# Performance work log

Hardware: AMD Instinct MI355X
Metric: run time of the kernel (lower is better)

## Reference

```python
import jax, jax.numpy as jnp
import numpy as np

DIM = 1024
NUM_ATT = 8
NUM_HEADS = 16
HEAD_DIM = DIM // NUM_HEADS
ROPE_BASE = 10000.0
NEG_INF = -1e9


def _rope(x):
    # x: [B, H, L, hd]; torchtune-style interleaved RoPE applied along the sequence axis.
    B, H, L, hd = x.shape
    pos = jnp.arange(L, dtype=jnp.float32)
    inv_freq = 1.0 / (ROPE_BASE ** (jnp.arange(0, hd, 2, dtype=jnp.float32) / hd))
    ang = pos[:, None] * inv_freq[None, :]          # [L, hd/2]
    cos = jnp.cos(ang)[None, None]                  # [1,1,L,hd/2]
    sin = jnp.sin(ang)[None, None]
    xr = x.reshape(B, H, L, hd // 2, 2)
    x0, x1 = xr[..., 0], xr[..., 1]
    out = jnp.stack([x0 * cos - x1 * sin, x1 * cos + x0 * sin], axis=-1)
    return out.reshape(B, H, L, hd).astype(x.dtype)


def setup_inputs() -> dict:
    key = jax.random.key(0)
    ks = jax.random.split(key, 7)
    B, L = 32, 512
    x = jax.random.normal(ks[0], (B, L, DIM), dtype=jnp.float32)
    s = 0.02  # init scale for numerical sanity (init choice, not math)
    query_projs = jax.random.normal(ks[1], (NUM_ATT, DIM, DIM), dtype=jnp.float32) * s
    key_projs = jax.random.normal(ks[2], (NUM_ATT, DIM, DIM), dtype=jnp.float32) * s
    value_projs = jax.random.normal(ks[3], (NUM_ATT, DIM, DIM), dtype=jnp.float32) * s
    out_projs = jax.random.normal(ks[4], (NUM_ATT, DIM, DIM), dtype=jnp.float32) * s
    router_w = jax.random.normal(ks[5], (DIM, NUM_ATT), dtype=jnp.float32) * s
    router_b = jnp.zeros((NUM_ATT,), dtype=jnp.float32)
    return {"x": x, "query_projs": query_projs, "key_projs": key_projs,
            "value_projs": value_projs, "out_projs": out_projs,
            "router_w": router_w, "router_b": router_b}


def reference(x, query_projs, key_projs, value_projs, out_projs, router_w, router_b):
    B, L, D = x.shape
    H, hd = NUM_HEADS, HEAD_DIM
    scale = hd ** -0.5

    # top-1 routing on mean-pooled tokens
    logits = x.mean(axis=1) @ router_w + router_b       # [B, E]
    attn_probs = jax.nn.softmax(logits, axis=-1)
    routes = jnp.argmax(attn_probs, axis=-1)            # [B] int

    # per-batch weight gather (the memory-bound irregular access) + bmm
    qw = query_projs[routes]                             # [B, D, D]
    kw = key_projs[routes]
    vw = value_projs[routes]
    q = jnp.einsum('bld,bde->ble', x, qw)
    k = jnp.einsum('bld,bde->ble', x, kw)
    v = jnp.einsum('bld,bde->ble', x, vw)

    q = q.reshape(B, L, H, hd).transpose(0, 2, 1, 3)     # [B,H,L,hd]
    k = k.reshape(B, L, H, hd).transpose(0, 2, 1, 3)
    v = v.reshape(B, L, H, hd).transpose(0, 2, 1, 3)

    q = _rope(q)
    k = _rope(k)

    scores = jnp.einsum('bhld,bhmd->bhlm', q, k) * scale  # [B,H,L,L]
    causal = jnp.triu(jnp.ones((L, L), dtype=bool), k=1)  # True above diag = masked
    scores = jnp.where(causal[None, None], NEG_INF, scores)
    attn = jax.nn.softmax(scores, axis=-1)
    out = jnp.einsum('bhlm,bhmd->bhld', attn, v)          # [B,H,L,hd]
    out = out.transpose(0, 2, 1, 3).reshape(B, L, D)

    ow = out_projs[routes]                                # [B, D, D]
    out = jnp.einsum('bld,bde->ble', out, ow)
    return out, attn_probs
```

## Files before the change

### kernel.cpp

```cpp
#include <hip/hip_runtime.h>


typedef __attribute__((ext_vector_type(8))) short bf16x8;
typedef __attribute__((ext_vector_type(4))) float f32x4;

typedef const __attribute__((address_space(1))) unsigned short* gas_t;
typedef __attribute__((address_space(3))) unsigned short* las_t;

#define OFF_PART   (0ull)
#define OFF_ROUTES (2ull << 20)
#define OFF_XB     (3ull << 20)
#define OFF_WT     (40ull << 20)
#define OFF_QKV    (112ull << 20)

__device__ __forceinline__ unsigned short f2bf(float f){
  unsigned int u = __float_as_uint(f);
  u += 0x7fffu + ((u >> 16) & 1u);
  return (unsigned short)(u >> 16);
}


__global__ void meanpool_kernel(const float* __restrict__ x, float* __restrict__ part,
                                unsigned short* __restrict__ xb){
  const int b = blockIdx.x, lc = blockIdx.y, t = threadIdx.x;
  const size_t base = ((size_t)b*512 + lc*32)*1024;
  const float* xs = x + base;
  unsigned short* xo = xb + base;
  float4 a = {0.f, 0.f, 0.f, 0.f};
  for (int l = 0; l < 32; ++l){
    const float4 v = *(const float4*)(xs + l*1024 + t*4);
    a.x += v.x; a.y += v.y; a.z += v.z; a.w += v.w;
    ushort4 pk;
    pk.x = f2bf(v.x); pk.y = f2bf(v.y); pk.z = f2bf(v.z); pk.w = f2bf(v.w);
    *(ushort4*)(xo + l*1024 + t*4) = pk;
  }
  *(float4*)(part + ((size_t)b*16 + lc)*1024 + t*4) = a;
}


__global__ void router_kernel(const float* __restrict__ part,
                              const float* __restrict__ rw,
                              const float* __restrict__ rbias,
                              float* __restrict__ probs,
                              int* __restrict__ routes){
  const int b = blockIdx.x, t = threadIdx.x;
  const int lane = t & 63, wave = t >> 6;
  __shared__ float wred[4][8];
  float p[8] = {0.f,0.f,0.f,0.f,0.f,0.f,0.f,0.f};
  #pragma unroll
  for (int k = 0; k < 4; ++k){
    const int d = t + k*256;
    float s = 0.f;
    #pragma unroll
    for (int lc = 0; lc < 16; ++lc)
      s += part[((size_t)b*16 + lc)*1024 + d];
    s *= (1.0f/512.0f);
    const float4 w0 = *(const float4*)(rw + d*8);
    const float4 w1 = *(const float4*)(rw + d*8 + 4);
    p[0] = fmaf(s, w0.x, p[0]); p[1] = fmaf(s, w0.y, p[1]);
    p[2] = fmaf(s, w0.z, p[2]); p[3] = fmaf(s, w0.w, p[3]);
    p[4] = fmaf(s, w1.x, p[4]); p[5] = fmaf(s, w1.y, p[5]);
    p[6] = fmaf(s, w1.z, p[6]); p[7] = fmaf(s, w1.w, p[7]);
  }
  #pragma unroll
  for (int off = 1; off < 64; off <<= 1)
    #pragma unroll
    for (int e = 0; e < 8; ++e)
      p[e] += __shfl_xor(p[e], off, 64);
  if (lane == 0){
    #pragma unroll
    for (int e = 0; e < 8; ++e) wred[wave][e] = p[e];
  }
  __syncthreads();
  if (t == 0){
    float lg[8], mx = -3e38f; int am = 0;
    #pragma unroll
    for (int e = 0; e < 8; ++e){
      lg[e] = wred[0][e] + wred[1][e] + wred[2][e] + wred[3][e] + rbias[e];
      if (lg[e] > mx){ mx = lg[e]; am = e; }
    }
    float sum = 0.f, ex[8];
    #pragma unroll
    for (int e = 0; e < 8; ++e){ ex[e] = __expf(lg[e] - mx); sum += ex[e]; }
    const float inv = 1.0f / sum;
    #pragma unroll
    for (int e = 0; e < 8; ++e) probs[b*8 + e] = ex[e] * inv;
    routes[b] = am;
  }
}


__global__ void wcast_kernel(const float* __restrict__ qw, const float* __restrict__ kw,
                             const float* __restrict__ vw, const float* __restrict__ ow,
                             unsigned short* __restrict__ Wt){
  __shared__ float tile[64][65];
  const int z = blockIdx.z;
  const float* Wm = (z < 8 ? qw : z < 16 ? kw : z < 24 ? vw : ow) + (size_t)(z & 7)*1024*1024;
  unsigned short* Wo = Wt + (size_t)z*1024*1024;
  const int t = threadIdx.x;
  const int r = t >> 4;
  const int c4 = t & 15;
  const int gx = blockIdx.x*64, gy = blockIdx.y*64;
  #pragma unroll
  for (int k = 0; k < 4; ++k){
    const int rr = r + 16*k;
    const float4 v = *(const float4*)(Wm + (size_t)(gy + rr)*1024 + gx + c4*4);
    tile[rr][c4*4+0] = v.x; tile[rr][c4*4+1] = v.y;
    tile[rr][c4*4+2] = v.z; tile[rr][c4*4+3] = v.w;
  }
  __syncthreads();
  #pragma unroll
  for (int k = 0; k < 4; ++k){
    const int rr = r + 16*k;
    ushort4 pk;
    pk.x = f2bf(tile[c4*4+0][rr]); pk.y = f2bf(tile[c4*4+1][rr]);
    pk.z = f2bf(tile[c4*4+2][rr]); pk.w = f2bf(tile[c4*4+3][rr]);
    *(ushort4*)(Wo + (size_t)(gx + rr)*1024 + gy + c4*4) = pk;
  }
}


template<int MODE>
__global__ __launch_bounds__(512, 2) void gemm_kernel(
    const unsigned short* __restrict__ A,
    const unsigned short* __restrict__ Wt,
    const int* __restrict__ routes,
    unsigned short* __restrict__ qkvout,
    float* __restrict__ outf,
    int pp)
{
  __shared__ __align__(16) unsigned short As[2][256*64];
  __shared__ __align__(16) unsigned short Bs[2][256*64];

  const int f = blockIdx.x + blockIdx.y*8;
  const int wg = (f & 7)*32 + (f >> 3);
  const int b    = wg >> 3;
  const int tile = wg & 7;
  const int m0 = (tile >> 2)*256;
  const int n0 = (tile & 3)*256;

  const int route = routes[b];
  const unsigned short* Ab = A + (size_t)b*512*1024;
  const unsigned short* Wb = Wt + (size_t)((MODE == 0) ? (pp*8 + route) : route)*1024*1024;

  const int t = threadIdx.x;
  const int lane = t & 63;
  const int wave = t >> 6;
  const int wm = (wave >> 2)*128;
  const int wn = (wave & 3)*64;
  const int quad = lane >> 4;
  const int ln = lane & 15;

  const int srow = t >> 3;
  const int schA = (t & 7) ^ (srow & 7);
  const int schB = (t & 7) ^ ((t >> 5) & 7);
  const unsigned short* gA0 = Ab + (size_t)(m0 + srow)*1024 + schA*8;
  const unsigned short* gB0 = Wb + (size_t)(n0 + srow)*1024 + schB*8;

  const int w8 = ln & 7;
  const int aO0 = (wm + ln)*64 + ((quad    ) ^ w8)*8;
  const int aO1 = (wm + ln)*64 + ((quad + 4) ^ w8)*8;
  const int bO0 = (wn + ln*4)*64 + ((quad    ) ^ w8)*8;
  const int bO1 = (wn + ln*4)*64 + ((quad + 4) ^ w8)*8;

  f32x4 acc[8][4] = {};
  bf16x8 a0[4][2], a1[4][2], b01[2][2], b23[2][2];

#define STAGE(c_, T_) do { \
    const size_t ko_ = (size_t)(T_)*64; \
    las_t dA_ = (las_t)(&As[c_][0]) + (size_t)t*8; \
    las_t dB_ = (las_t)(&Bs[c_][0]) + (size_t)t*8; \
    _Pragma("unroll") \
    for (int k_ = 0; k_ < 4; ++k_){ \
      __builtin_amdgcn_global_load_lds((gas_t)(gA0 + ko_ + (size_t)k_*65536), dA_ + k_*4096, 16, 0, 0); \
      __builtin_amdgcn_global_load_lds((gas_t)(gB0 + ko_ + (size_t)k_*65536), dB_ + k_*4096, 16, 0, 0); \
    } \
  } while (0)

#define RD(ptr_, off_) (*(const bf16x8*)((ptr_) + (off_)))
#define READ_F0(pA_, pB_) do { \
    _Pragma("unroll") for (int f_ = 0; f_ < 4; ++f_){ \
      a0[f_][0] = RD(pA_, aO0 + f_*1024); a0[f_][1] = RD(pA_, aO1 + f_*1024); } \
    _Pragma("unroll") for (int f_ = 0; f_ < 2; ++f_){ \
      b01[f_][0] = RD(pB_, bO0 + f_*64); b01[f_][1] = RD(pB_, bO1 + f_*64); } \
  } while (0)
#define READ_F1(pA_) do { \
    _Pragma("unroll") for (int f_ = 0; f_ < 4; ++f_){ \
      a1[f_][0] = RD(pA_, aO0 + (4+f_)*1024); a1[f_][1] = RD(pA_, aO1 + (4+f_)*1024); } \
  } while (0)
#define READ_F2(pB_) do { \
    _Pragma("unroll") for (int f_ = 0; f_ < 2; ++f_){ \
      b23[f_][0] = RD(pB_, bO0 + (2+f_)*64); b23[f_][1] = RD(pB_, bO1 + (2+f_)*64); } \
  } while (0)

#define MSET(AF_, BF_, IB_, JB_) do { \
    _Pragma("unroll") for (int f_ = 0; f_ < 4; ++f_) \
    _Pragma("unroll") for (int n_ = 0; n_ < 2; ++n_) \
    _Pragma("unroll") for (int k_ = 0; k_ < 2; ++k_) \
      acc[IB_+f_][JB_+n_] = __builtin_amdgcn_mfma_f32_16x16x32_bf16( \
          AF_[f_][k_], BF_[n_][k_], acc[IB_+f_][JB_+n_], 0, 0, 0); \
  } while (0)

  STAGE(0, 0);
  STAGE(1, 1);
  asm volatile("s_waitcnt vmcnt(8)" ::: "memory");
  __builtin_amdgcn_s_barrier();
  READ_F0((&As[0][0]), (&Bs[0][0]));

  for (int g = 0; g < 16; ++g){
    const int c = g & 1;
    const unsigned short* pA  = &As[c][0];
    const unsigned short* pB  = &Bs[c][0];
    const unsigned short* pAn = &As[c ^ 1][0];
    const unsigned short* pBn = &Bs[c ^ 1][0];

    READ_F1(pA);
    __builtin_amdgcn_s_barrier();
    asm volatile("s_waitcnt lgkmcnt(8)" ::: "memory");
    __builtin_amdgcn_sched_barrier(0);
    __builtin_amdgcn_s_setprio(1);
    MSET(a0, b01, 0, 0);
    __builtin_amdgcn_s_setprio(0);
    __builtin_amdgcn_s_barrier();

    READ_F2(pB);
    __builtin_amdgcn_s_barrier();
    asm volatile("s_waitcnt lgkmcnt(4)" ::: "memory");
    __builtin_amdgcn_sched_barrier(0);
    __builtin_amdgcn_s_setprio(1);
    MSET(a1, b01, 4, 0);
    __builtin_amdgcn_s_setprio(0);
    __builtin_amdgcn_s_barrier();

    asm volatile("s_waitcnt lgkmcnt(0)" ::: "memory");
    __builtin_amdgcn_sched_barrier(0);
    __builtin_amdgcn_s_setprio(1);
    MSET(a1, b23, 4, 2);
    __builtin_amdgcn_s_setprio(0);
    __builtin_amdgcn_s_barrier();

    if (g < 14){
      STAGE(c, g + 2);
      asm volatile("s_waitcnt vmcnt(8)" ::: "memory");
    } else if (g == 14){
      asm volatile("s_waitcnt vmcnt(0)" ::: "memory");
    }
    __builtin_amdgcn_s_barrier();
    __builtin_amdgcn_s_setprio(1);
    MSET(a0, b23, 0, 2);
    __builtin_amdgcn_s_setprio(0);
    if (g < 15) READ_F0(pAn, pBn);
    __builtin_amdgcn_s_barrier();
  }
#undef STAGE
#undef RD
#undef READ_F0
#undef READ_F1
#undef READ_F2
#undef MSET

  if (MODE == 0){
    const size_t PSZ = (size_t)32*16*512*64;
    const int h = (n0 + wn) >> 6;
    if (pp < 2){
      const int eh0 = ln*4;
      const float invf0 = exp2f(-0.41524101f * (float)(ln*2));
      const float invf1 = invf0 * 0.74989420832f;
      float sc0, cc0, sc1, cc1;
      __sincosf(invf0, &sc0, &cc0);
      __sincosf(invf1, &sc1, &cc1);
      unsigned short* outp = qkvout + ((((size_t)pp*32 + b)*16 + h)*512)*64 + eh0;
      #pragma unroll
      for (int fm = 0; fm < 8; ++fm){
        const int l0 = m0 + wm + fm*16 + quad*4;
        float s0, c0, s1, c1;
        __sincosf((float)l0 * invf0, &s0, &c0);
        __sincosf((float)l0 * invf1, &s1, &c1);
        #pragma unroll
        for (int r = 0; r < 4; ++r){
          const int l = l0 + r;
          const float x0 = acc[fm][0][r], x1 = acc[fm][1][r];
          const float x2 = acc[fm][2][r], x3 = acc[fm][3][r];
          ushort4 pk;
          pk.x = f2bf(x0*c0 - x1*s0);
          pk.y = f2bf(x1*c0 + x0*s0);
          pk.z = f2bf(x2*c1 - x3*s1);
          pk.w = f2bf(x3*c1 + x2*s1);
          *(ushort4*)(outp + (size_t)l*64) = pk;
          const float nc0 = c0*cc0 - s0*sc0, ns0 = s0*cc0 + c0*sc0;
          const float nc1 = c1*cc1 - s1*sc1, ns1 = s1*cc1 + c1*sc1;
          c0 = nc0; s0 = ns0; c1 = nc1; s1 = ns1;
        }
      }
    } else {
      #pragma unroll
      for (int fn = 0; fn < 4; ++fn){
        const int eh = ln*4 + fn;
        unsigned short* outp = qkvout + 2*PSZ + (((size_t)b*16 + h)*64 + eh)*512;
        #pragma unroll
        for (int fm = 0; fm < 8; ++fm){
          const int l0 = m0 + wm + fm*16 + quad*4;
          ushort4 pk;
          pk.x = f2bf(acc[fm][fn][0]); pk.y = f2bf(acc[fm][fn][1]);
          pk.z = f2bf(acc[fm][fn][2]); pk.w = f2bf(acc[fm][fn][3]);
          *(ushort4*)(outp + l0) = pk;
        }
      }
    }
  } else {
    const int e0 = n0 + wn + ln*4;
    #pragma unroll
    for (int fm = 0; fm < 8; ++fm){
      #pragma unroll
      for (int r = 0; r < 4; ++r){
        const int l = m0 + wm + fm*16 + quad*4 + r;
        float4 f4;
        f4.x = acc[fm][0][r]; f4.y = acc[fm][1][r];
        f4.z = acc[fm][2][r]; f4.w = acc[fm][3][r];
        *(float4*)(outf + ((size_t)b*512 + l)*1024 + e0) = f4;
      }
    }
  }
}


#define PSTR 72

__global__ __launch_bounds__(256, 3) void attn_kernel(
    const unsigned short* __restrict__ qkv,
    unsigned short* __restrict__ ctx)
{
  __shared__ __align__(16) unsigned short Ks[2][64*64];
  __shared__ __align__(16) unsigned short Vts[2][64*64];
  __shared__ __align__(16) unsigned short Ps[4][32*PSTR];

  const int qt = blockIdx.x, h = blockIdx.y, b = blockIdx.z;

  const size_t HO  = (((size_t)b)*16 + h)*512*64;
  const size_t PSZ = (size_t)32*16*512*64;
  const unsigned short* Qg  = qkv + HO;
  const unsigned short* Kg  = qkv + PSZ + HO;
  const unsigned short* Vtg = qkv + 2*PSZ + HO;

  const int t    = threadIdx.x;
  const int lane = t & 63;
  const int wave = t >> 6;
  const int quad = lane >> 4;
  const int ln   = lane & 15;

  const int u0 = t, u1 = t + 256;
  const int kr0 = u0 >> 3, kc0 = (u0 & 7) ^ (kr0 & 7);
  const int kr1 = u1 >> 3, kc1 = (u1 & 7) ^ (kr1 & 7);

  bf16x8 aq[2][2];
  #pragma unroll
  for (int rg = 0; rg < 2; ++rg){
    const int row = qt*128 + rg*64 + wave*16 + ln;
    #pragma unroll
    for (int ks = 0; ks < 2; ++ks)
      aq[rg][ks] = *(const bf16x8*)(Qg + (size_t)row*64 + ks*32 + quad*8);
  }

  const int ktEnd = 2*qt + 1;

  __builtin_amdgcn_global_load_lds((gas_t)(Kg  + kr0*64  + kc0*8), (las_t)(Ks[0]  + u0*8), 16,0,0);
  __builtin_amdgcn_global_load_lds((gas_t)(Kg  + kr1*64  + kc1*8), (las_t)(Ks[0]  + u1*8), 16,0,0);
  __builtin_amdgcn_global_load_lds((gas_t)(Vtg + kr0*512 + kc0*8), (las_t)(Vts[0] + u0*8), 16,0,0);
  __builtin_amdgcn_global_load_lds((gas_t)(Vtg + kr1*512 + kc1*8), (las_t)(Vts[0] + u1*8), 16,0,0);

  float m_r[2][4], l_r[2][4];
  #pragma unroll
  for (int rg = 0; rg < 2; ++rg)
    #pragma unroll
    for (int r = 0; r < 4; ++r){ m_r[rg][r] = -3e38f; l_r[rg][r] = 0.f; }
  f32x4 o[2][4] = {};

  const int swzl = ln & 7;
  unsigned short* Pw = Ps[wave];
  const int rowoff = wave*16 + quad*4;

  for (int kt = 0; kt <= ktEnd; ++kt){
    __syncthreads();
    if (kt < ktEnd){
      const unsigned short* Kn  = Kg + (kt+1)*4096;
      const int col = (kt+1)*64;
      unsigned short* kb = Ks[(kt+1)&1];
      unsigned short* vb = Vts[(kt+1)&1];
      __builtin_amdgcn_global_load_lds((gas_t)(Kn  + kr0*64 + kc0*8),        (las_t)(kb + u0*8), 16,0,0);
      __builtin_amdgcn_global_load_lds((gas_t)(Kn  + kr1*64 + kc1*8),        (las_t)(kb + u1*8), 16,0,0);
      __builtin_amdgcn_global_load_lds((gas_t)(Vtg + kr0*512 + col + kc0*8), (las_t)(vb + u0*8), 16,0,0);
      __builtin_amdgcn_global_load_lds((gas_t)(Vtg + kr1*512 + col + kc1*8), (las_t)(vb + u1*8), 16,0,0);
    }
    const unsigned short* ks_ = Ks[kt&1];
    const unsigned short* vt_ = Vts[kt&1];

    #pragma unroll
    for (int rg = 0; rg < 2; ++rg){
      if (rg == 0 && kt > 2*qt) continue;
      const bool diag = (kt == 2*qt + rg);

      f32x4 s[4] = {};
      __builtin_amdgcn_s_setprio(1);
      #pragma unroll
      for (int ks2 = 0; ks2 < 2; ++ks2){
        #pragma unroll
        for (int kn = 0; kn < 4; ++kn){
          const bf16x8 bk = *(const bf16x8*)(ks_ + (kn*16+ln)*64 + (((quad + ks2*4) ^ swzl))*8);
          s[kn] = __builtin_amdgcn_mfma_f32_16x16x32_bf16(aq[rg][ks2], bk, s[kn], 0, 0, 0);
        }
      }
      __builtin_amdgcn_s_setprio(0);

      float p[4][4], lm[4] = {-3e38f,-3e38f,-3e38f,-3e38f};
      #pragma unroll
      for (int kn = 0; kn < 4; ++kn){
        const int col = kn*16 + ln;
        #pragma unroll
        for (int r = 0; r < 4; ++r){
          float v = s[kn][r] * 0.125f;
          if (diag && col > rowoff + r) v = -1e9f;
          p[kn][r] = v;
          lm[r] = fmaxf(lm[r], v);
        }
      }
      #pragma unroll
      for (int off = 1; off < 16; off <<= 1)
        #pragma unroll
        for (int r = 0; r < 4; ++r)
          lm[r] = fmaxf(lm[r], __shfl_xor(lm[r], off, 64));
      float alpha[4], rsum[4];
      #pragma unroll
      for (int r = 0; r < 4; ++r){
        const float mn = fmaxf(m_r[rg][r], lm[r]);
        alpha[r] = __expf(m_r[rg][r] - mn);
        m_r[rg][r] = mn;
      }
      #pragma unroll
      for (int kn = 0; kn < 4; ++kn)
        #pragma unroll
        for (int r = 0; r < 4; ++r)
          p[kn][r] = __expf(p[kn][r] - m_r[rg][r]);
      #pragma unroll
      for (int r = 0; r < 4; ++r)
        rsum[r] = (p[0][r] + p[1][r]) + (p[2][r] + p[3][r]);
      #pragma unroll
      for (int off = 1; off < 16; off <<= 1)
        #pragma unroll
        for (int r = 0; r < 4; ++r)
          rsum[r] += __shfl_xor(rsum[r], off, 64);
      #pragma unroll
      for (int r = 0; r < 4; ++r) l_r[rg][r] = l_r[rg][r]*alpha[r] + rsum[r];
      #pragma unroll
      for (int dn = 0; dn < 4; ++dn)
        #pragma unroll
        for (int r = 0; r < 4; ++r)
          o[rg][dn][r] *= alpha[r];

      #pragma unroll
      for (int kn = 0; kn < 4; ++kn)
        #pragma unroll
        for (int r = 0; r < 4; ++r)
          Pw[(rg*16 + quad*4 + r)*PSTR + kn*16 + ln] = f2bf(p[kn][r]);

      __builtin_amdgcn_s_setprio(1);
      #pragma unroll
      for (int ks2 = 0; ks2 < 2; ++ks2){
        const bf16x8 ap = *(const bf16x8*)(Pw + (rg*16 + ln)*PSTR + quad*8 + ks2*32);
        #pragma unroll
        for (int dn = 0; dn < 4; ++dn){
          const bf16x8 bv = *(const bf16x8*)(vt_ + (dn*16+ln)*64 + (((quad + ks2*4) ^ swzl))*8);
          o[rg][dn] = __builtin_amdgcn_mfma_f32_16x16x32_bf16(ap, bv, o[rg][dn], 0, 0, 0);
        }
      }
      __builtin_amdgcn_s_setprio(0);
    }
  }

  #pragma unroll
  for (int rg = 0; rg < 2; ++rg){
    #pragma unroll
    for (int r = 0; r < 4; ++r){
      const float inv = 1.0f / l_r[rg][r];
      const int row = qt*128 + rg*64 + wave*16 + quad*4 + r;
      unsigned short* op = ctx + ((size_t)b*512 + row)*1024 + h*64 + ln;
      #pragma unroll
      for (int dn = 0; dn < 4; ++dn)
        op[dn*16] = f2bf(o[rg][dn][r] * inv);
    }
  }
}


extern "C" void kernel_launch(void* const* d_in, const int* in_sizes, int n_in,
                              void* d_out, int out_size, void* d_ws, size_t ws_size,
                              hipStream_t stream) {
  const float* x     = (const float*)d_in[0];
  const float* qw    = (const float*)d_in[1];
  const float* kw    = (const float*)d_in[2];
  const float* vw    = (const float*)d_in[3];
  const float* ow    = (const float*)d_in[4];
  const float* rw    = (const float*)d_in[5];
  const float* rbias = (const float*)d_in[6];
  float* out = (float*)d_out;
  char* ws = (char*)d_ws;

  float* part            = (float*)(ws + OFF_PART);
  int* routes            = (int*)(ws + OFF_ROUTES);
  unsigned short* xb     = (unsigned short*)(ws + OFF_XB);
  unsigned short* wt     = (unsigned short*)(ws + OFF_WT);
  unsigned short* qkvbuf = (unsigned short*)(ws + OFF_QKV);
  unsigned short* ctx    = xb;
  float* probs = out + (size_t)32*512*1024;

  meanpool_kernel<<<dim3(32, 16), 256, 0, stream>>>(x, part, xb);
  router_kernel<<<32, 256, 0, stream>>>(part, rw, rbias, probs, routes);
  wcast_kernel<<<dim3(16, 16, 32), 256, 0, stream>>>(qw, kw, vw, ow, wt);
  gemm_kernel<0><<<dim3(8, 32), 512, 0, stream>>>(xb, wt, routes, qkvbuf, nullptr, 0);
  gemm_kernel<0><<<dim3(8, 32), 512, 0, stream>>>(xb, wt, routes, qkvbuf, nullptr, 1);
  gemm_kernel<0><<<dim3(8, 32), 512, 0, stream>>>(xb, wt, routes, qkvbuf, nullptr, 2);
  attn_kernel<<<dim3(4, 16, 32), 256, 0, stream>>>(qkvbuf, ctx);
  gemm_kernel<1><<<dim3(8, 32), 512, 0, stream>>>(ctx, wt + (size_t)24*1024*1024, routes,
                                                  nullptr, out, 0);
}
```

Baseline: 509.8 us.

## Pair causal query tiles per block for balanced attention work and shared K/V loads

Each attention block now handles two query tiles of the same (batch, head), pairing tile 3-pr with tile pr. Every block then does the same total number of causal K/V tile iterations, and each K/V tile loaded into LDS is reused by both query tiles. The grid becomes 1D with 1024 blocks, and block indices are remapped with an interleaved (f&7)*128 swizzle, probably for XCD placement. The cost is doubled accumulator and Q register state (o, m, l, aq), which may raise VGPR pressure and reduce occupancy under launch_bounds(256,3).

```diff
diff --git a/kernel.cpp b/kernel.cpp
--- a/kernel.cpp
+++ b/kernel.cpp
@@ -334,7 +334,14 @@
   __shared__ __align__(16) unsigned short Vts[2][64*64];
   __shared__ __align__(16) unsigned short Ps[4][32*PSTR];
 
-  const int qt = blockIdx.x, h = blockIdx.y, b = blockIdx.z;
+  const int f = blockIdx.x;
+  const int l = (f & 7)*128 + (f >> 3);
+  const int pr = l & 1;
+  const int h  = (l >> 1) & 15;
+  const int b  = l >> 5;
+
+  const int qts[2] = {3 - pr, pr};
+  const int ktEnd = 2*qts[0] + 1;
 
   const size_t HO  = (((size_t)b)*16 + h)*512*64;
   const size_t PSZ = (size_t)32*16*512*64;
@@ -352,28 +359,30 @@
   const int kr0 = u0 >> 3, kc0 = (u0 & 7) ^ (kr0 & 7);
   const int kr1 = u1 >> 3, kc1 = (u1 & 7) ^ (kr1 & 7);
 
-  bf16x8 aq[2][2];
-  #pragma unroll
-  for (int rg = 0; rg < 2; ++rg){
-    const int row = qt*128 + rg*64 + wave*16 + ln;
-    #pragma unroll
-    for (int ks = 0; ks < 2; ++ks)
-      aq[rg][ks] = *(const bf16x8*)(Qg + (size_t)row*64 + ks*32 + quad*8);
-  }
-
-  const int ktEnd = 2*qt + 1;
+  bf16x8 aq[2][2][2];
+  #pragma unroll
+  for (int tau = 0; tau < 2; ++tau)
+    #pragma unroll
+    for (int rg = 0; rg < 2; ++rg){
+      const int row = qts[tau]*128 + rg*64 + wave*16 + ln;
+      #pragma unroll
+      for (int ks = 0; ks < 2; ++ks)
+        aq[tau][rg][ks] = *(const bf16x8*)(Qg + (size_t)row*64 + ks*32 + quad*8);
+    }
 
   __builtin_amdgcn_global_load_lds((gas_t)(Kg  + kr0*64  + kc0*8), (las_t)(Ks[0]  + u0*8), 16,0,0);
   __builtin_amdgcn_global_load_lds((gas_t)(Kg  + kr1*64  + kc1*8), (las_t)(Ks[0]  + u1*8), 16,0,0);
   __builtin_amdgcn_global_load_lds((gas_t)(Vtg + kr0*512 + kc0*8), (las_t)(Vts[0] + u0*8), 16,0,0);
   __builtin_amdgcn_global_load_lds((gas_t)(Vtg + kr1*512 + kc1*8), (las_t)(Vts[0] + u1*8), 16,0,0);
 
-  float m_r[2][4], l_r[2][4];
-  #pragma unroll
-  for (int rg = 0; rg < 2; ++rg)
-    #pragma unroll
-    for (int r = 0; r < 4; ++r){ m_r[rg][r] = -3e38f; l_r[rg][r] = 0.f; }
-  f32x4 o[2][4] = {};
+  float m_r[2][2][4], l_r[2][2][4];
+  #pragma unroll
+  for (int tau = 0; tau < 2; ++tau)
+    #pragma unroll
+    for (int rg = 0; rg < 2; ++rg)
+      #pragma unroll
+      for (int r = 0; r < 4; ++r){ m_r[tau][rg][r] = -3e38f; l_r[tau][rg][r] = 0.f; }
+  f32x4 o[2][2][4] = {};
 
   const int swzl = ln & 7;
   unsigned short* Pw = Ps[wave];
@@ -395,99 +404,107 @@
     const unsigned short* vt_ = Vts[kt&1];
 
     #pragma unroll
+    for (int tau = 0; tau < 2; ++tau){
+      const int qt = qts[tau];
+      if (kt > 2*qt + 1) continue;
+
+      #pragma unroll
+      for (int rg = 0; rg < 2; ++rg){
+        if (rg == 0 && kt > 2*qt) continue;
+        const bool diag = (kt == 2*qt + rg);
+
+        f32x4 s[4] = {};
+        __builtin_amdgcn_s_setprio(1);
+        #pragma unroll
+        for (int ks2 = 0; ks2 < 2; ++ks2){
+          #pragma unroll
+          for (int kn = 0; kn < 4; ++kn){
+            const bf16x8 bk = *(const bf16x8*)(ks_ + (kn*16+ln)*64 + (((quad + ks2*4) ^ swzl))*8);
+            s[kn] = __builtin_amdgcn_mfma_f32_16x16x32_bf16(aq[tau][rg][ks2], bk, s[kn], 0, 0, 0);
+          }
+        }
+        __builtin_amdgcn_s_setprio(0);
+
+        float p[4][4], lm[4] = {-3e38f,-3e38f,-3e38f,-3e38f};
+        #pragma unroll
+        for (int kn = 0; kn < 4; ++kn){
+          const int col = kn*16 + ln;
+          #pragma unroll
+          for (int r = 0; r < 4; ++r){
+            float v = s[kn][r] * 0.125f;
+            if (diag && col > rowoff + r) v = -1e9f;
+            p[kn][r] = v;
+            lm[r] = fmaxf(lm[r], v);
+          }
+        }
+        #pragma unroll
+        for (int off = 1; off < 16; off <<= 1)
+          #pragma unroll
+          for (int r = 0; r < 4; ++r)
+            lm[r] = fmaxf(lm[r], __shfl_xor(lm[r], off, 64));
+        float alpha[4], rsum[4];
+        #pragma unroll
+        for (int r = 0; r < 4; ++r){
+          const float mn = fmaxf(m_r[tau][rg][r], lm[r]);
+          alpha[r] = __expf(m_r[tau][rg][r] - mn);
+          m_r[tau][rg][r] = mn;
+        }
+        #pragma unroll
+        for (int kn = 0; kn < 4; ++kn)
+          #pragma unroll
+          for (int r = 0; r < 4; ++r)
+            p[kn][r] = __expf(p[kn][r] - m_r[tau][rg][r]);
+        #pragma unroll
+        for (int r = 0; r < 4; ++r)
+          rsum[r] = (p[0][r] + p[1][r]) + (p[2][r] + p[3][r]);
+        #pragma unroll
+        for (int off = 1; off < 16; off <<= 1)
+          #pragma unroll
+          for (int r = 0; r < 4; ++r)
+            rsum[r] += __shfl_xor(rsum[r], off, 64);
+        #pragma unroll
+        for (int r = 0; r < 4; ++r) l_r[tau][rg][r] = l_r[tau][rg][r]*alpha[r] + rsum[r];
+        #pragma unroll
+        for (int dn = 0; dn < 4; ++dn)
+          #pragma unroll
+          for (int r = 0; r < 4; ++r)
+            o[tau][rg][dn][r] *= alpha[r];
+
+        #pragma unroll
+        for (int kn = 0; kn < 4; ++kn)
+          #pragma unroll
+          for (int r = 0; r < 4; ++r)
+            Pw[(rg*16 + quad*4 + r)*PSTR + kn*16 + ln] = f2bf(p[kn][r]);
+
+        __builtin_amdgcn_s_setprio(1);
+        #pragma unroll
+        for (int ks2 = 0; ks2 < 2; ++ks2){
+          const bf16x8 ap = *(const bf16x8*)(Pw + (rg*16 + ln)*PSTR + quad*8 + ks2*32);
+          #pragma unroll
+          for (int dn = 0; dn < 4; ++dn){
+            const bf16x8 bv = *(const bf16x8*)(vt_ + (dn*16+ln)*64 + (((quad + ks2*4) ^ swzl))*8);
+            o[tau][rg][dn] = __builtin_amdgcn_mfma_f32_16x16x32_bf16(ap, bv, o[tau][rg][dn], 0, 0, 0);
+          }
+        }
+        __builtin_amdgcn_s_setprio(0);
+      }
+    }
+  }
+
+  #pragma unroll
+  for (int tau = 0; tau < 2; ++tau)
+    #pragma unroll
     for (int rg = 0; rg < 2; ++rg){
-      if (rg == 0 && kt > 2*qt) continue;
-      const bool diag = (kt == 2*qt + rg);
-
-      f32x4 s[4] = {};
-      __builtin_amdgcn_s_setprio(1);
-      #pragma unroll
-      for (int ks2 = 0; ks2 < 2; ++ks2){
-        #pragma unroll
-        for (int kn = 0; kn < 4; ++kn){
-          const bf16x8 bk = *(const bf16x8*)(ks_ + (kn*16+ln)*64 + (((quad + ks2*4) ^ swzl))*8);
-          s[kn] = __builtin_amdgcn_mfma_f32_16x16x32_bf16(aq[rg][ks2], bk, s[kn], 0, 0, 0);
-        }
+      #pragma unroll
+      for (int r = 0; r < 4; ++r){
+        const float inv = 1.0f / l_r[tau][rg][r];
+        const int row = qts[tau]*128 + rg*64 + wave*16 + quad*4 + r;
+        unsigned short* op = ctx + ((size_t)b*512 + row)*1024 + h*64 + ln;
+        #pragma unroll
+        for (int dn = 0; dn < 4; ++dn)
+          op[dn*16] = f2bf(o[tau][rg][dn][r] * inv);
       }
-      __builtin_amdgcn_s_setprio(0);
-
-      float p[4][4], lm[4] = {-3e38f,-3e38f,-3e38f,-3e38f};
-      #pragma unroll
-      for (int kn = 0; kn < 4; ++kn){
-        const int col = kn*16 + ln;
-        #pragma unroll
-        for (int r = 0; r < 4; ++r){
-          float v = s[kn][r] * 0.125f;
-          if (diag && col > rowoff + r) v = -1e9f;
-          p[kn][r] = v;
-          lm[r] = fmaxf(lm[r], v);
-        }
-      }
-      #pragma unroll
-      for (int off = 1; off < 16; off <<= 1)
-        #pragma unroll
-        for (int r = 0; r < 4; ++r)
-          lm[r] = fmaxf(lm[r], __shfl_xor(lm[r], off, 64));
-      float alpha[4], rsum[4];
-      #pragma unroll
-      for (int r = 0; r < 4; ++r){
-        const float mn = fmaxf(m_r[rg][r], lm[r]);
-        alpha[r] = __expf(m_r[rg][r] - mn);
-        m_r[rg][r] = mn;
-      }
-      #pragma unroll
-      for (int kn = 0; kn < 4; ++kn)
-        #pragma unroll
-        for (int r = 0; r < 4; ++r)
-          p[kn][r] = __expf(p[kn][r] - m_r[rg][r]);
-      #pragma unroll
-      for (int r = 0; r < 4; ++r)
-        rsum[r] = (p[0][r] + p[1][r]) + (p[2][r] + p[3][r]);
-      #pragma unroll
-      for (int off = 1; off < 16; off <<= 1)
-        #pragma unroll
-        for (int r = 0; r < 4; ++r)
-          rsum[r] += __shfl_xor(rsum[r], off, 64);
-      #pragma unroll
-      for (int r = 0; r < 4; ++r) l_r[rg][r] = l_r[rg][r]*alpha[r] + rsum[r];
-      #pragma unroll
-      for (int dn = 0; dn < 4; ++dn)
-        #pragma unroll
-        for (int r = 0; r < 4; ++r)
-          o[rg][dn][r] *= alpha[r];
-
-      #pragma unroll
-      for (int kn = 0; kn < 4; ++kn)
-        #pragma unroll
-        for (int r = 0; r < 4; ++r)
-          Pw[(rg*16 + quad*4 + r)*PSTR + kn*16 + ln] = f2bf(p[kn][r]);
-
-      __builtin_amdgcn_s_setprio(1);
-      #pragma unroll
-      for (int ks2 = 0; ks2 < 2; ++ks2){
-        const bf16x8 ap = *(const bf16x8*)(Pw + (rg*16 + ln)*PSTR + quad*8 + ks2*32);
-        #pragma unroll
-        for (int dn = 0; dn < 4; ++dn){
-          const bf16x8 bv = *(const bf16x8*)(vt_ + (dn*16+ln)*64 + (((quad + ks2*4) ^ swzl))*8);
-          o[rg][dn] = __builtin_amdgcn_mfma_f32_16x16x32_bf16(ap, bv, o[rg][dn], 0, 0, 0);
-        }
-      }
-      __builtin_amdgcn_s_setprio(0);
-    }
-  }
-
-  #pragma unroll
-  for (int rg = 0; rg < 2; ++rg){
-    #pragma unroll
-    for (int r = 0; r < 4; ++r){
-      const float inv = 1.0f / l_r[rg][r];
-      const int row = qt*128 + rg*64 + wave*16 + quad*4 + r;
-      unsigned short* op = ctx + ((size_t)b*512 + row)*1024 + h*64 + ln;
-      #pragma unroll
-      for (int dn = 0; dn < 4; ++dn)
-        op[dn*16] = f2bf(o[rg][dn][r] * inv);
-    }
-  }
+    }
 }
 
 
@@ -518,7 +535,7 @@
   gemm_kernel<0><<<dim3(8, 32), 512, 0, stream>>>(xb, wt, routes, qkvbuf, nullptr, 0);
   gemm_kernel<0><<<dim3(8, 32), 512, 0, stream>>>(xb, wt, routes, qkvbuf, nullptr, 1);
   gemm_kernel<0><<<dim3(8, 32), 512, 0, stream>>>(xb, wt, routes, qkvbuf, nullptr, 2);
-  attn_kernel<<<dim3(4, 16, 32), 256, 0, stream>>>(qkvbuf, ctx);
+  attn_kernel<<<1024, 256, 0, stream>>>(qkvbuf, ctx);
   gemm_kernel<1><<<dim3(8, 32), 512, 0, stream>>>(ctx, wt + (size_t)24*1024*1024, routes,
                                                   nullptr, out, 0);
 }
```

Result: no change. 515.7 us (+1.2%).
